# Kernel optimization log

Measured on AMD Instinct MI355X. Metric: run time of the kernel, lower is better.

The kernel has to match this reference:

```python
import jax, jax.numpy as jnp
import numpy as np

N_QUBITS = 8
N_LAYERS = 4


def setup_inputs() -> dict:
    key = jax.random.key(0)
    k_x, k_rot, k_ent, k_w, k_b = jax.random.split(key, 5)
    B, S, F = 64, 8192, 64
    x = jax.random.normal(k_x, (B, S, F), dtype=jnp.float32)
    rotation_params = jax.random.normal(k_rot, (N_LAYERS, N_QUBITS, 3), dtype=jnp.float32) * 0.01
    entangle_params = jax.random.normal(k_ent, (N_LAYERS, N_QUBITS - 1), dtype=jnp.float32) * 0.01
    proj_w = jax.random.normal(k_w, (N_QUBITS * 2, N_QUBITS), dtype=jnp.float32) * (1.0 / np.sqrt(N_QUBITS))
    proj_b = jax.random.normal(k_b, (N_QUBITS * 2,), dtype=jnp.float32) * 0.01
    return {"x": x, "rotation_params": rotation_params, "entangle_params": entangle_params,
            "proj_w": proj_w, "proj_b": proj_b}


def reference(x, rotation_params, entangle_params, proj_w, proj_b):
    n_layers, n_qubits, _ = rotation_params.shape
    # amplitude encoding: tanh of first n_qubits features -> [B, S, Q]
    qs = jnp.tanh(x[..., :n_qubits])
    for layer in range(n_layers):
        r = rotation_params[layer]  # [Q, 3]
        # rx, ry, rz are each (cos+sin)*state -> fused per-qubit scale
        scale = ((jnp.cos(r[:, 0]) + jnp.sin(r[:, 0]))
                 * (jnp.cos(r[:, 1]) + jnp.sin(r[:, 1]))
                 * (jnp.cos(r[:, 2]) + jnp.sin(r[:, 2])))  # [Q]
        rz = qs * scale  # broadcast over [B, S, Q]
        # entanglement: entangled[..., i] = rz[i]*(1-w_i) + rz[i+1]*w_i, last qubit unchanged
        w = jax.nn.sigmoid(entangle_params[layer])  # [Q-1]
        front = rz[..., :-1] * (1.0 - w) + rz[..., 1:] * w
        qs = jnp.concatenate([front, rz[..., -1:]], axis=-1)
    # projection Linear(Q -> 2Q)
    return jnp.einsum('bsq,oq->bso', qs, proj_w) + proj_b
```

## Files before the change

### kernel.cpp

```cpp
#include <hip/hip_runtime.h>

#define NQ 8
#define NL 4
#define NO 16

typedef __attribute__((ext_vector_type(4))) float float4v;

__global__ __launch_bounds__(256) void qcl_fused(
    const float* __restrict__ x,
    const float* __restrict__ rot,
    const float* __restrict__ ent,
    const float* __restrict__ pw,
    const float* __restrict__ pb,
    float* __restrict__ out,
    int n_rows)
{
    __shared__ float sScale[NL][NQ];
    __shared__ float sWl[NL][NQ - 1];
    __shared__ float sW[NO][NQ];
    __shared__ float sB[NO];

    const int tid = threadIdx.x;

    const int nhalf = n_rows * 2;
    const int H = gridDim.x * 256;
    const int gid = blockIdx.x * 256 + tid;
    const int h = tid & 1;

    int g[4];
    bool v[4];
    #pragma unroll
    for (int k = 0; k < 4; ++k) { g[k] = gid + k * H; v[k] = g[k] < nhalf; }

    float4v a[4];
    #pragma unroll
    for (int k = 0; k < 4; ++k) {
        a[k] = float4v{0.f, 0.f, 0.f, 0.f};
        if (v[k]) a[k] = *(const float4v*)(x + (size_t)(g[k] >> 1) * 64 + h * 4);
    }

    if (tid < NL * NQ) {
        const int l = tid >> 3, q = tid & 7;
        const float r0 = rot[(l * NQ + q) * 3 + 0];
        const float r1 = rot[(l * NQ + q) * 3 + 1];
        const float r2 = rot[(l * NQ + q) * 3 + 2];
        sScale[l][q] = (__cosf(r0) + __sinf(r0)) *
                       (__cosf(r1) + __sinf(r1)) *
                       (__cosf(r2) + __sinf(r2));
    } else if (tid < NL * NQ + NL * (NQ - 1)) {
        const int u = tid - NL * NQ;
        const int l = u / 7, i = u - l * 7;
        const float e = __expf(-ent[l * 7 + i]);
        sWl[l][i] = __builtin_amdgcn_rcpf(1.0f + e);
    } else if (tid >= 64 && tid < 64 + NO) {
        sB[tid - 64] = pb[tid - 64];
    }
    __syncthreads();

    if (tid < NO) {
        float W[NQ];
        #pragma unroll
        for (int q = 0; q < NQ; ++q) W[q] = pw[tid * NQ + q];
        #pragma unroll
        for (int l = NL - 1; l >= 0; --l) {
            float WE[NQ];
            WE[0] = W[0] * (1.0f - sWl[l][0]);
            #pragma unroll
            for (int j = 1; j < NQ - 1; ++j)
                WE[j] = W[j] * (1.0f - sWl[l][j]) + W[j - 1] * sWl[l][j - 1];
            WE[NQ - 1] = W[NQ - 1] + W[NQ - 2] * sWl[l][NQ - 2];
            #pragma unroll
            for (int q = 0; q < NQ; ++q) W[q] = WE[q] * sScale[l][q];
        }
        #pragma unroll
        for (int q = 0; q < NQ; ++q) sW[tid][q] = W[q];
    }
    __syncthreads();

    float m[4][4];
    #pragma unroll
    for (int k = 0; k < 4; ++k) {
        #pragma unroll
        for (int j = 0; j < 4; ++j) {
            float e = __expf(2.0f * a[k][j]);
            m[k][j] = 1.0f - 2.0f * __builtin_amdgcn_rcpf(e + 1.0f);
        }
    }

    float t[4][8];
    #pragma unroll
    for (int k = 0; k < 4; ++k) {
        #pragma unroll
        for (int j = 0; j < 4; ++j) {
            float o = __shfl_xor(m[k][j], 1, 64);
            t[k][j]     = h ? o : m[k][j];
            t[k][j + 4] = h ? m[k][j] : o;
        }
    }

    const int base = h * 8;
    const float4v* wrow = (const float4v*)&sW[base][0];
    float acc[4][8];
    #pragma unroll
    for (int j = 0; j < 8; ++j) {
        float4v w0 = wrow[2 * j];
        float4v w1 = wrow[2 * j + 1];
        float bj = sB[base + j];
        #pragma unroll
        for (int k = 0; k < 4; ++k) {
            acc[k][j] = bj
                + w0.x * t[k][0] + w0.y * t[k][1] + w0.z * t[k][2] + w0.w * t[k][3]
                + w1.x * t[k][4] + w1.y * t[k][5] + w1.z * t[k][6] + w1.w * t[k][7];
        }
    }

    #pragma unroll
    for (int k = 0; k < 4; ++k) {
        if (v[k]) {
            float4v* p = (float4v*)(out + (size_t)(g[k] >> 1) * 16 + base);
            float4v u0 = {acc[k][0], acc[k][1], acc[k][2], acc[k][3]};
            float4v u1 = {acc[k][4], acc[k][5], acc[k][6], acc[k][7]};
            __builtin_nontemporal_store(u0, p);
            __builtin_nontemporal_store(u1, p + 1);
        }
    }
}

extern "C" void kernel_launch(void* const* d_in, const int* in_sizes, int n_in,
                              void* d_out, int out_size, void* d_ws, size_t ws_size,
                              hipStream_t stream) {
    const float* x   = (const float*)d_in[0];
    const float* rot = (const float*)d_in[1];
    const float* ent = (const float*)d_in[2];
    const float* pw  = (const float*)d_in[3];
    const float* pb  = (const float*)d_in[4];
    float* out = (float*)d_out;

    const int n_rows = in_sizes[0] / 64;
    const int nhalf = n_rows * 2;
    const int block = 256;
    const int grid = (nhalf + block * 4 - 1) / (block * 4);
    hipLaunchKernelGGL(qcl_fused, dim3(grid), dim3(block), 0, stream,
                       x, rot, ent, pw, pb, out, n_rows);
}
```

Measured before the change: 28.64 us.

## Load whole x rows with dense coalesced wave loads and redistribute via shuffles

```diff
diff --git a/kernel.cpp b/kernel.cpp
--- a/kernel.cpp
+++ b/kernel.cpp
@@ -6,7 +6,7 @@
 
 typedef __attribute__((ext_vector_type(4))) float float4v;
 
-__global__ __launch_bounds__(256) void qcl_fused(
+__global__ __launch_bounds__(256) void qcl_dense(
     const float* __restrict__ x,
     const float* __restrict__ rot,
     const float* __restrict__ ent,
@@ -20,23 +20,23 @@
     __shared__ float sW[NO][NQ];
     __shared__ float sB[NO];
 
-    const int tid = threadIdx.x;
+    const int tid  = threadIdx.x;
+    const int lane = tid & 63;
+    const int wglob = blockIdx.x * 4 + (tid >> 6);
+    const int R0 = wglob * 64;
+    const int R1 = R0 + 32;
+    const int h    = lane & 1;
+    const int krow = lane >> 1;
 
-    const int nhalf = n_rows * 2;
-    const int H = gridDim.x * 256;
-    const int gid = blockIdx.x * 256 + tid;
-    const int h = tid & 1;
+    const float4v* xb = (const float4v*)x;
+    const size_t last4 = (size_t)n_rows * 16 - 1;
 
-    int g[4];
-    bool v[4];
+    float4v s[8];
     #pragma unroll
-    for (int k = 0; k < 4; ++k) { g[k] = gid + k * H; v[k] = g[k] < nhalf; }
-
-    float4v a[4];
-    #pragma unroll
-    for (int k = 0; k < 4; ++k) {
-        a[k] = float4v{0.f, 0.f, 0.f, 0.f};
-        if (v[k]) a[k] = *(const float4v*)(x + (size_t)(g[k] >> 1) * 64 + h * 4);
+    for (int i = 0; i < 8; ++i) {
+        size_t fidx = (size_t)R0 * 16 + i * 64 + lane;
+        if (fidx > last4) fidx = last4;
+        s[i] = xb[fidx];
     }
 
     if (tid < NL * NQ) {
@@ -77,49 +77,62 @@
     }
     __syncthreads();
 
-    float m[4][4];
+    const int srcLane = ((lane >> 1) & 3) * 16 + h;
+    const int myreg = lane >> 3;
+    const int base = h * 8;
+    const float4v* wrow = (const float4v*)&sW[base][0];
+
     #pragma unroll
-    for (int k = 0; k < 4; ++k) {
+    for (int tt = 0; tt < 2; ++tt) {
+        float c0 = 0.f, c1 = 0.f, c2 = 0.f, c3 = 0.f;
+        #pragma unroll
+        for (int r = 0; r < 8; ++r) {
+            float f0 = __shfl(s[r][0], srcLane, 64);
+            float f1 = __shfl(s[r][1], srcLane, 64);
+            float f2 = __shfl(s[r][2], srcLane, 64);
+            float f3 = __shfl(s[r][3], srcLane, 64);
+            if (myreg == r) { c0 = f0; c1 = f1; c2 = f2; c3 = f3; }
+        }
+
+        if (tt == 0) {
+            #pragma unroll
+            for (int i = 0; i < 8; ++i) {
+                size_t fidx = (size_t)R1 * 16 + i * 64 + lane;
+                if (fidx > last4) fidx = last4;
+                s[i] = xb[fidx];
+            }
+        }
+
+        float m[4], cc[4] = {c0, c1, c2, c3};
         #pragma unroll
         for (int j = 0; j < 4; ++j) {
-            float e = __expf(2.0f * a[k][j]);
-            m[k][j] = 1.0f - 2.0f * __builtin_amdgcn_rcpf(e + 1.0f);
+            float e = __expf(2.0f * cc[j]);
+            m[j] = 1.0f - 2.0f * __builtin_amdgcn_rcpf(e + 1.0f);
         }
-    }
 
-    float t[4][8];
-    #pragma unroll
-    for (int k = 0; k < 4; ++k) {
+        float t[8];
         #pragma unroll
         for (int j = 0; j < 4; ++j) {
-            float o = __shfl_xor(m[k][j], 1, 64);
-            t[k][j]     = h ? o : m[k][j];
-            t[k][j + 4] = h ? m[k][j] : o;
+            float o = __shfl_xor(m[j], 1, 64);
+            t[j]     = h ? o : m[j];
+            t[j + 4] = h ? m[j] : o;
         }
-    }
 
-    const int base = h * 8;
-    const float4v* wrow = (const float4v*)&sW[base][0];
-    float acc[4][8];
-    #pragma unroll
-    for (int j = 0; j < 8; ++j) {
-        float4v w0 = wrow[2 * j];
-        float4v w1 = wrow[2 * j + 1];
-        float bj = sB[base + j];
+        float acc[8];
         #pragma unroll
-        for (int k = 0; k < 4; ++k) {
-            acc[k][j] = bj
-                + w0.x * t[k][0] + w0.y * t[k][1] + w0.z * t[k][2] + w0.w * t[k][3]
-                + w1.x * t[k][4] + w1.y * t[k][5] + w1.z * t[k][6] + w1.w * t[k][7];
+        for (int j = 0; j < 8; ++j) {
+            float4v w0 = wrow[2 * j];
+            float4v w1 = wrow[2 * j + 1];
+            acc[j] = sB[base + j]
+                + w0[0] * t[0] + w0[1] * t[1] + w0[2] * t[2] + w0[3] * t[3]
+                + w1[0] * t[4] + w1[1] * t[5] + w1[2] * t[6] + w1[3] * t[7];
         }
-    }
 
-    #pragma unroll
-    for (int k = 0; k < 4; ++k) {
-        if (v[k]) {
-            float4v* p = (float4v*)(out + (size_t)(g[k] >> 1) * 16 + base);
-            float4v u0 = {acc[k][0], acc[k][1], acc[k][2], acc[k][3]};
-            float4v u1 = {acc[k][4], acc[k][5], acc[k][6], acc[k][7]};
+        const int row = (tt == 0 ? R0 : R1) + krow;
+        if (row < n_rows) {
+            float4v* p = (float4v*)(out + (size_t)row * 16 + base);
+            float4v u0 = {acc[0], acc[1], acc[2], acc[3]};
+            float4v u1 = {acc[4], acc[5], acc[6], acc[7]};
             __builtin_nontemporal_store(u0, p);
             __builtin_nontemporal_store(u1, p + 1);
         }
@@ -137,9 +150,9 @@
     float* out = (float*)d_out;
 
     const int n_rows = in_sizes[0] / 64;
-    const int nhalf = n_rows * 2;
+    const int waves = (n_rows + 63) / 64;
     const int block = 256;
-    const int grid = (nhalf + block * 4 - 1) / (block * 4);
-    hipLaunchKernelGGL(qcl_fused, dim3(grid), dim3(block), 0, stream,
+    const int grid = (waves + 3) / 4;
+    hipLaunchKernelGGL(qcl_dense, dim3(grid), dim3(block), 0, stream,
                        x, rot, ent, pw, pb, out, n_rows);
 }
```

New measurement: 32.97 us. +15.1%, slower.
